# Optimization experiments

Measured on AMD Instinct MI355X. Metric: run time of the kernel, lower is better.

The kernel has to match this reference:

```python
import jax, jax.numpy as jnp
import numpy as np

EMBED = 2048
HIDDEN = 2048
LENGTH = 8192


def setup_inputs() -> dict:
    key = jax.random.key(0)
    ks = jax.random.split(key, 7)
    s = 1.0 / np.sqrt(HIDDEN)
    x = jax.random.normal(ks[0], (1, LENGTH, EMBED), dtype=jnp.float32)
    # PyTorch-style GRUCell params: gates ordered (r, z, n) along leading dim
    W_ih = jax.random.uniform(ks[1], (3 * HIDDEN, EMBED), jnp.float32, -s, s)
    W_hh = jax.random.uniform(ks[2], (3 * HIDDEN, HIDDEN), jnp.float32, -s, s)
    b_ih = jax.random.uniform(ks[3], (3 * HIDDEN,), jnp.float32, -s, s)
    b_hh = jax.random.uniform(ks[4], (3 * HIDDEN,), jnp.float32, -s, s)
    fc_w = jax.random.uniform(ks[5], (1, HIDDEN), jnp.float32, -s, s)
    fc_b = jax.random.uniform(ks[6], (1,), jnp.float32, -s, s)
    return {"x": x, "W_ih": W_ih, "W_hh": W_hh, "b_ih": b_ih, "b_hh": b_hh,
            "fc_w": fc_w, "fc_b": fc_b}


def reference(x, W_ih, W_hh, b_ih, b_hh, fc_w, fc_b):
    # x: [1, L, E]; sequential GRU over L timesteps, then linear + sigmoid ('Score' mode)
    H = W_hh.shape[1]

    def cell(h, xt):
        # xt: [1, E], h: [1, H]
        gi = xt @ W_ih.T + b_ih            # [1, 3H]
        gh = h @ W_hh.T + b_hh             # [1, 3H]
        i_r, i_z, i_n = jnp.split(gi, 3, axis=-1)
        h_r, h_z, h_n = jnp.split(gh, 3, axis=-1)
        r = jax.nn.sigmoid(i_r + h_r)
        z = jax.nn.sigmoid(i_z + h_z)
        n = jnp.tanh(i_n + r * h_n)
        h_new = (1.0 - z) * n + z * h
        return h_new, None

    h0 = jnp.zeros((1, H), dtype=x.dtype)
    xs = jnp.swapaxes(x, 0, 1)             # [L, 1, E] for scan over time
    hT, _ = jax.lax.scan(cell, h0, xs)
    out = jax.nn.sigmoid(hT @ fc_w.T + fc_b)  # [1, 1]
    return out
```

## Files before the change

### kernel.cpp

```cpp
#include <hip/hip_runtime.h>
#include <hip/hip_bf16.h>
#include <cstdint>

#define L_SEQ 8192
#define EMB   2048
#define HID   2048
#define N3H   6144

typedef __attribute__((ext_vector_type(8))) short short8;
typedef __attribute__((ext_vector_type(4))) float f32x4;
typedef __attribute__((ext_vector_type(4))) unsigned int uintx4;

__device__ __forceinline__ unsigned short f2bf(float f) {
    union { float f; unsigned int u; } v; v.f = f;
    unsigned int u = v.u;
    unsigned int lsb = (u >> 16) & 1u;
    u += 0x7fffu + lsb;
    return (unsigned short)(u >> 16);
}

__device__ __forceinline__ float bf2f(unsigned int s) {
    union { unsigned int u; float f; } v;
    v.u = (s & 0xffffu) << 16;
    return v.f;
}

__device__ __forceinline__ uintx4 ld16(const uintx4* p) {
    uintx4 r;
    asm volatile("global_load_dwordx4 %0, %1, off sc0 sc1\n\ts_waitcnt vmcnt(0)"
                 : "=v"(r) : "v"(p) : "memory");
    return r;
}
__device__ __forceinline__ void st16(uintx4* p, uintx4 v) {
    asm volatile("global_store_dwordx4 %0, %1, off sc0 sc1"
                 :: "v"(p), "v"(v) : "memory");
}

__global__ void cvt_f32_bf16(const float* __restrict__ src,
                             unsigned short* __restrict__ dst, int n) {
    int i = (blockIdx.x * blockDim.x + threadIdx.x) * 4;
    if (i < n) {
        float4 v = *(const float4*)(src + i);
        ushort4 o;
        o.x = f2bf(v.x); o.y = f2bf(v.y); o.z = f2bf(v.z); o.w = f2bf(v.w);
        *(ushort4*)(dst + i) = o;
    }
}

__global__ __launch_bounds__(256) void gemm_gi(const unsigned short* __restrict__ Xb,
                                               const unsigned short* __restrict__ Wb,
                                               const float* __restrict__ bih,
                                               unsigned short* __restrict__ GIb) {
    __shared__ unsigned short As[128][40];
    __shared__ unsigned short Bs[128][40];
    const int tid = threadIdx.x;
    const int wid = tid >> 6, l = tid & 63;
    const int q = l >> 4, r16 = l & 15;
    const int bm = blockIdx.y, bn = blockIdx.x;
    const int wm = (wid >> 1) * 64, wn = (wid & 1) * 64;

    f32x4 acc[4][4] = {};

    const int srow = tid >> 1, sseg = (tid & 1) * 16;
    const unsigned short* xsrc = Xb + (size_t)(bm * 128 + srow) * 2048 + sseg;
    const unsigned short* wsrc = Wb + (size_t)(bn * 128 + srow) * 2048 + sseg;

    for (int k0 = 0; k0 < 2048; k0 += 32) {
        __syncthreads();
        uint4 va0 = *(const uint4*)(xsrc + k0);
        uint4 va1 = *(const uint4*)(xsrc + k0 + 8);
        uint4 vb0 = *(const uint4*)(wsrc + k0);
        uint4 vb1 = *(const uint4*)(wsrc + k0 + 8);
        *(uint4*)&As[srow][sseg]     = va0;
        *(uint4*)&As[srow][sseg + 8] = va1;
        *(uint4*)&Bs[srow][sseg]     = vb0;
        *(uint4*)&Bs[srow][sseg + 8] = vb1;
        __syncthreads();

        short8 af[4], bfr[4];
#pragma unroll
        for (int i = 0; i < 4; i++) af[i]  = *(const short8*)&As[wm + 16 * i + r16][q * 8];
#pragma unroll
        for (int j = 0; j < 4; j++) bfr[j] = *(const short8*)&Bs[wn + 16 * j + r16][q * 8];
#pragma unroll
        for (int i = 0; i < 4; i++)
#pragma unroll
            for (int j = 0; j < 4; j++)
                acc[i][j] = __builtin_amdgcn_mfma_f32_16x16x32_bf16(af[i], bfr[j], acc[i][j], 0, 0, 0);
    }

#pragma unroll
    for (int j = 0; j < 4; j++) {
        int n = bn * 128 + wn + 16 * j + r16;
        float bias = bih[n];
#pragma unroll
        for (int i = 0; i < 4; i++) {
            int mbase = bm * 128 + wm + 16 * i + q * 4;
#pragma unroll
            for (int p = 0; p < 4; p++) {
                GIb[(size_t)(mbase + p) * N3H + n] = f2bf(acc[i][j][p] + bias);
            }
        }
    }
}

__global__ __launch_bounds__(512, 2) void gru_scan(const float* __restrict__ Whh,
                                                   const float* __restrict__ bhh,
                                                   const unsigned short* __restrict__ GIb,
                                                   uintx4* rec,
                                                   unsigned int* cnt) {
    __shared__ float h_lds[2][2048];
    __shared__ float hnew_lds[8];
    const int tid = threadIdx.x;
    const int w = tid >> 6, l = tid & 63;
    const int b = blockIdx.x;
    const int hidx = b * 8 + w;

    float4 wreg[3][8];
    float bb[3];
#pragma unroll
    for (int g = 0; g < 3; g++) {
        int r = g * HID + hidx;
        bb[g] = bhh[r];
        const float* wr = Whh + (size_t)r * HID + 4 * l;
#pragma unroll
        for (int i = 0; i < 8; i++) wreg[g][i] = *(const float4*)(wr + 256 * i);
    }

    {
        float4 z4 = {0.f, 0.f, 0.f, 0.f};
        *(float4*)&h_lds[0][tid * 4] = z4;
    }
    __syncthreads();

    unsigned short gr = GIb[hidx];
    unsigned short gz = GIb[2048 + hidx];
    unsigned short gn = GIb[4096 + hidx];

    for (int t = 0; t < L_SEQ; t++) {
        const int p = t & 1;

        unsigned short gr2 = 0, gz2 = 0, gn2 = 0;
        if (t + 1 < L_SEQ) {
            const unsigned short* gq = GIb + (size_t)(t + 1) * N3H + hidx;
            gr2 = gq[0]; gz2 = gq[2048]; gn2 = gq[4096];
        }

        if (t > 0) {
            const unsigned int tgt = 32u * (unsigned)((t + (t & 1)) >> 1);
            if (w == 0) {
                while (1) {
                    unsigned int c = tgt;
                    if (l < 8)
                        c = __hip_atomic_load(&cnt[(size_t)p * 128 + l * 16],
                                              __ATOMIC_RELAXED, __HIP_MEMORY_SCOPE_AGENT);
                    if (__all(c >= tgt)) break;
                }
            }
            __syncthreads();

            const uintx4* rp = rec + (size_t)p * 512 + tid;
            uintx4 rv = ld16(rp);
            while (rv.z != (unsigned int)t) rv = ld16(rp);
            float4 hv;
            hv.x = bf2f(rv.x);
            hv.y = bf2f(rv.x >> 16);
            hv.z = bf2f(rv.y);
            hv.w = bf2f(rv.y >> 16);
            *(float4*)&h_lds[p][4 * tid] = hv;
        }
        __syncthreads();

        float hprev = h_lds[p][hidx];

        float a0 = 0.f, a1 = 0.f, a2 = 0.f;
#pragma unroll
        for (int i = 0; i < 8; i++) {
            float4 hv = *(const float4*)&h_lds[p][4 * l + 256 * i];
            a0 = fmaf(wreg[0][i].x, hv.x, a0); a0 = fmaf(wreg[0][i].y, hv.y, a0);
            a0 = fmaf(wreg[0][i].z, hv.z, a0); a0 = fmaf(wreg[0][i].w, hv.w, a0);
            a1 = fmaf(wreg[1][i].x, hv.x, a1); a1 = fmaf(wreg[1][i].y, hv.y, a1);
            a1 = fmaf(wreg[1][i].z, hv.z, a1); a1 = fmaf(wreg[1][i].w, hv.w, a1);
            a2 = fmaf(wreg[2][i].x, hv.x, a2); a2 = fmaf(wreg[2][i].y, hv.y, a2);
            a2 = fmaf(wreg[2][i].z, hv.z, a2); a2 = fmaf(wreg[2][i].w, hv.w, a2);
        }
        a0 += __shfl_xor(a0, 32); a1 += __shfl_xor(a1, 32); a2 += __shfl_xor(a2, 32);
        a0 += __shfl_xor(a0, 16); a1 += __shfl_xor(a1, 16); a2 += __shfl_xor(a2, 16);
        a0 += __shfl_xor(a0, 8);  a1 += __shfl_xor(a1, 8);  a2 += __shfl_xor(a2, 8);
        a0 += __shfl_xor(a0, 4);  a1 += __shfl_xor(a1, 4);  a2 += __shfl_xor(a2, 4);
        a0 += __shfl_xor(a0, 2);  a1 += __shfl_xor(a1, 2);  a2 += __shfl_xor(a2, 2);
        a0 += __shfl_xor(a0, 1);  a1 += __shfl_xor(a1, 1);  a2 += __shfl_xor(a2, 1);

        if (l == 0) {
            float r  = 1.f / (1.f + __expf(-(bf2f(gr) + a0 + bb[0])));
            float z  = 1.f / (1.f + __expf(-(bf2f(gz) + a1 + bb[1])));
            float hn = a2 + bb[2];
            float xn = bf2f(gn) + r * hn;
            xn = fminf(fmaxf(xn, -15.f), 15.f);
            float e  = __expf(2.f * xn);
            float nn = (e - 1.f) / (e + 1.f);
            hnew_lds[w] = z * hprev + (1.f - z) * nn;
        }
        __syncthreads();

        if (tid < 2) {
            const float* hp = hnew_lds + 4 * tid;
            unsigned int w0 = (unsigned int)f2bf(hp[0]) | ((unsigned int)f2bf(hp[1]) << 16);
            unsigned int w1 = (unsigned int)f2bf(hp[2]) | ((unsigned int)f2bf(hp[3]) << 16);
            uintx4 pk;
            pk.x = w0; pk.y = w1; pk.z = (unsigned int)(t + 1); pk.w = 0u;
            st16(rec + (size_t)((t + 1) & 1) * 512 + 2 * b + tid, pk);
        }
        if (tid == 0)
            __hip_atomic_fetch_add(&cnt[(size_t)((t + 1) & 1) * 128 + (b & 7) * 16], 1u,
                                   __ATOMIC_RELAXED, __HIP_MEMORY_SCOPE_AGENT);

        gr = gr2; gz = gz2; gn = gn2;
    }
}

__global__ void fc_out(const uintx4* __restrict__ rec,
                       const float* __restrict__ fw,
                       const float* __restrict__ fb, float* __restrict__ out) {
    __shared__ float red[8];
    const int tid = threadIdx.x;
    const int wid = tid >> 6, l = tid & 63;
    uintx4 rv = *(rec + tid);
    float4 wv = *(const float4*)&fw[4 * tid];
    float s = bf2f(rv.x) * wv.x + bf2f(rv.x >> 16) * wv.y +
              bf2f(rv.y) * wv.z + bf2f(rv.y >> 16) * wv.w;
    s += __shfl_xor(s, 32); s += __shfl_xor(s, 16); s += __shfl_xor(s, 8);
    s += __shfl_xor(s, 4);  s += __shfl_xor(s, 2);  s += __shfl_xor(s, 1);
    if (l == 0) red[wid] = s;
    __syncthreads();
    if (tid == 0) {
        float tot = 0.f;
#pragma unroll
        for (int i = 0; i < 8; i++) tot += red[i];
        tot += fb[0];
        out[0] = 1.f / (1.f + __expf(-tot));
    }
}

extern "C" void kernel_launch(void* const* d_in, const int* in_sizes, int n_in,
                              void* d_out, int out_size, void* d_ws, size_t ws_size,
                              hipStream_t stream) {
    const float* x   = (const float*)d_in[0];
    const float* Wih = (const float*)d_in[1];
    const float* Whh = (const float*)d_in[2];
    const float* bih = (const float*)d_in[3];
    const float* bhh = (const float*)d_in[4];
    const float* fcw = (const float*)d_in[5];
    const float* fcb = (const float*)d_in[6];
    float* out = (float*)d_out;

    char* ws = (char*)d_ws;
    unsigned short* Xb  = (unsigned short*)ws;
    unsigned short* Wb  = (unsigned short*)(ws + 33554432);
    unsigned short* GIb = (unsigned short*)(ws + 58720256);
    uintx4* rec         = (uintx4*)(ws + 159383552);
    unsigned int* cnt   = (unsigned int*)(ws + 159399936);

    hipMemsetAsync(cnt, 0, 1024, stream);

    cvt_f32_bf16<<<16384, 256, 0, stream>>>(x,   Xb, L_SEQ * EMB);
    cvt_f32_bf16<<<12288, 256, 0, stream>>>(Wih, Wb, N3H * EMB);

    dim3 gg(48, 64);
    gemm_gi<<<gg, 256, 0, stream>>>(Xb, Wb, bih, GIb);

    gru_scan<<<256, 512, 0, stream>>>(Whh, bhh, GIb, rec, cnt);

    fc_out<<<1, 512, 0, stream>>>(rec, fcw, fcb, out);
}
```

Baseline: 23.21 ms.

## Replace atomic counter barrier with per-block tag flags polled by vector loads

```diff
diff --git a/kernel.cpp b/kernel.cpp
--- a/kernel.cpp
+++ b/kernel.cpp
@@ -33,6 +33,10 @@
 }
 __device__ __forceinline__ void st16(uintx4* p, uintx4 v) {
     asm volatile("global_store_dwordx4 %0, %1, off sc0 sc1"
+                 :: "v"(p), "v"(v) : "memory");
+}
+__device__ __forceinline__ void st4(unsigned int* p, unsigned int v) {
+    asm volatile("global_store_dword %0, %1, off sc0 sc1"
                  :: "v"(p), "v"(v) : "memory");
 }
 
@@ -104,11 +108,11 @@
     }
 }
 
-__global__ __launch_bounds__(512, 2) void gru_scan(const float* __restrict__ Whh,
+__global__ __launch_bounds__(512, 1) void gru_scan(const float* __restrict__ Whh,
                                                    const float* __restrict__ bhh,
                                                    const unsigned short* __restrict__ GIb,
                                                    uintx4* rec,
-                                                   unsigned int* cnt) {
+                                                   unsigned int* tags) {
     __shared__ float h_lds[2][2048];
     __shared__ float hnew_lds[8];
     const int tid = threadIdx.x;
@@ -147,14 +151,13 @@
         }
 
         if (t > 0) {
-            const unsigned int tgt = 32u * (unsigned)((t + (t & 1)) >> 1);
             if (w == 0) {
+                const uintx4* tp = (const uintx4*)(tags + (size_t)p * 256) + l;
+                const unsigned int tg = (unsigned int)t;
                 while (1) {
-                    unsigned int c = tgt;
-                    if (l < 8)
-                        c = __hip_atomic_load(&cnt[(size_t)p * 128 + l * 16],
-                                              __ATOMIC_RELAXED, __HIP_MEMORY_SCOPE_AGENT);
-                    if (__all(c >= tgt)) break;
+                    uintx4 tv = ld16(tp);
+                    int ok = (tv.x == tg) & (tv.y == tg) & (tv.z == tg) & (tv.w == tg);
+                    if (__all(ok)) break;
                 }
             }
             __syncthreads();
@@ -203,17 +206,19 @@
         }
         __syncthreads();
 
-        if (tid < 2) {
-            const float* hp = hnew_lds + 4 * tid;
-            unsigned int w0 = (unsigned int)f2bf(hp[0]) | ((unsigned int)f2bf(hp[1]) << 16);
-            unsigned int w1 = (unsigned int)f2bf(hp[2]) | ((unsigned int)f2bf(hp[3]) << 16);
-            uintx4 pk;
-            pk.x = w0; pk.y = w1; pk.z = (unsigned int)(t + 1); pk.w = 0u;
-            st16(rec + (size_t)((t + 1) & 1) * 512 + 2 * b + tid, pk);
-        }
-        if (tid == 0)
-            __hip_atomic_fetch_add(&cnt[(size_t)((t + 1) & 1) * 128 + (b & 7) * 16], 1u,
-                                   __ATOMIC_RELAXED, __HIP_MEMORY_SCOPE_AGENT);
+        if (w == 0) {
+            if (l < 2) {
+                const float* hp = hnew_lds + 4 * l;
+                unsigned int w0 = (unsigned int)f2bf(hp[0]) | ((unsigned int)f2bf(hp[1]) << 16);
+                unsigned int w1 = (unsigned int)f2bf(hp[2]) | ((unsigned int)f2bf(hp[3]) << 16);
+                uintx4 pk;
+                pk.x = w0; pk.y = w1; pk.z = (unsigned int)(t + 1); pk.w = 0u;
+                st16(rec + (size_t)((t + 1) & 1) * 512 + 2 * b + l, pk);
+            }
+            asm volatile("s_waitcnt vmcnt(0)" ::: "memory");
+            if (l == 0)
+                st4(tags + (size_t)((t + 1) & 1) * 256 + b, (unsigned int)(t + 1));
+        }
 
         gr = gr2; gz = gz2; gn = gn2;
     }
@@ -259,9 +264,7 @@
     unsigned short* Wb  = (unsigned short*)(ws + 33554432);
     unsigned short* GIb = (unsigned short*)(ws + 58720256);
     uintx4* rec         = (uintx4*)(ws + 159383552);
-    unsigned int* cnt   = (unsigned int*)(ws + 159399936);
-
-    hipMemsetAsync(cnt, 0, 1024, stream);
+    unsigned int* tags  = (unsigned int*)(ws + 159399936);
 
     cvt_f32_bf16<<<16384, 256, 0, stream>>>(x,   Xb, L_SEQ * EMB);
     cvt_f32_bf16<<<12288, 256, 0, stream>>>(Wih, Wb, N3H * EMB);
@@ -269,7 +272,7 @@
     dim3 gg(48, 64);
     gemm_gi<<<gg, 256, 0, stream>>>(Xb, Wb, bih, GIb);
 
-    gru_scan<<<256, 512, 0, stream>>>(Whh, bhh, GIb, rec, cnt);
+    gru_scan<<<256, 512, 0, stream>>>(Whh, bhh, GIb, rec, tags);
 
     fc_out<<<1, 512, 0, stream>>>(rec, fcw, fcb, out);
 }
```

New measurement: 25.01 ms. 7.7% more time.
